# Optimization experiments

Measured on AMD Instinct MI355X. Metric: run time of the kernel, lower is better.

The kernel has to match this reference:

```python
import jax, jax.numpy as jnp
import numpy as np

N = 100000   # nodes
E = 1600000  # edges
B = 64       # graphs
NI, EI, GI = 64, 32, 32   # node_in, edge_in, global_in
NO, EO, GO = 32, 32, 32   # node_out, edge_out, global_out
H = 3                     # attention heads
NEG_SLOPE = 0.2


def setup_inputs() -> dict:
    key = jax.random.key(0)
    ks = jax.random.split(key, 20)
    s = 0.1
    return {
        # graph data
        "x": jax.random.normal(ks[0], (N, NI), jnp.float32),
        "edge_attr": jax.random.normal(ks[1], (E, EI), jnp.float32),
        "glob": jax.random.normal(ks[2], (B, GI), jnp.float32),
        # edge_mlp: Lin(node_in+edge_in, edge_out)
        "W_edge": jax.random.normal(ks[3], (NI + EI, EO), jnp.float32) * s,
        "b_edge": jax.random.normal(ks[4], (EO,), jnp.float32) * s,
        # GATv2Conv params (heads=3, edge_dim=EO)
        "W_l": jax.random.normal(ks[5], (NI, H * NO), jnp.float32) * s,
        "b_l": jax.random.normal(ks[6], (H * NO,), jnp.float32) * s,
        "W_r": jax.random.normal(ks[7], (NI, H * NO), jnp.float32) * s,
        "b_r": jax.random.normal(ks[8], (H * NO,), jnp.float32) * s,
        "W_e": jax.random.normal(ks[9], (EO, H * NO), jnp.float32) * s,   # lin_edge (no bias)
        "att": jax.random.normal(ks[10], (H, NO), jnp.float32) * s,
        "bias_gat": jax.random.normal(ks[11], (H * NO,), jnp.float32) * s,
        # node_mlp_2: Lin(node_out*3 + global_in, node_out)
        "W_n2": jax.random.normal(ks[12], (H * NO + GI, NO), jnp.float32) * s,
        "b_n2": jax.random.normal(ks[13], (NO,), jnp.float32) * s,
        # global_mlp: Lin(global_in + node_out, global_out)
        "W_g": jax.random.normal(ks[14], (GI + NO, GO), jnp.float32) * s,
        "b_g": jax.random.normal(ks[15], (GO,), jnp.float32) * s,
        # int inputs
        "edge_index": jax.random.randint(ks[16], (2, E), 0, N, jnp.int32),
        "batch": jnp.sort(jax.random.randint(ks[17], (N,), 0, B, jnp.int32)),
    }


def reference(x, edge_attr, glob, W_edge, b_edge, W_l, b_l, W_r, b_r, W_e,
              att, bias_gat, W_n2, b_n2, W_g, b_g, edge_index, batch):
    src, dst = edge_index[0], edge_index[1]

    # --- edge model: relu(Lin([x[src], edge_attr])) ---
    e = jax.nn.relu(jnp.concatenate([x[src], edge_attr], axis=1) @ W_edge + b_edge)  # [E, EO]

    # --- node model: GATv2Conv(heads=3, edge_dim=EO), concat heads ---
    xl = (x @ W_l + b_l).reshape(N, H, NO)   # source transform
    xr = (x @ W_r + b_r).reshape(N, H, NO)   # target transform
    m = xl[src] + xr[dst] + (e @ W_e).reshape(E, H, NO)          # [E,H,NO]
    logits = (jax.nn.leaky_relu(m, NEG_SLOPE) * att).sum(-1)     # [E,H]
    # segment softmax over incoming edges of each target node
    mx = jax.ops.segment_max(logits, dst, num_segments=N)        # [N,H]
    ex = jnp.exp(logits - mx[dst])
    den = jax.ops.segment_sum(ex, dst, num_segments=N)           # [N,H]
    alpha = ex / den[dst]                                        # [E,H]
    msg = (alpha[..., None] * xl[src]).reshape(E, H * NO)
    gat_out = jax.ops.segment_sum(msg, dst, num_segments=N) + bias_gat  # [N, H*NO]
    x_new = jax.nn.relu(jnp.concatenate([gat_out, glob[batch]], axis=1) @ W_n2 + b_n2)  # [N,NO]

    # --- global model: relu(Lin([glob, scatter_mean(x_new, batch)])) ---
    cnt = jax.ops.segment_sum(jnp.ones((N,), x.dtype), batch, num_segments=B)
    mean = jax.ops.segment_sum(x_new, batch, num_segments=B) / jnp.maximum(cnt, 1.0)[:, None]
    u_new = jax.nn.relu(jnp.concatenate([glob, mean], axis=1) @ W_g + b_g)  # [B,GO]

    return x_new, e, u_new
```

## Files before the change

kernel.cpp:

```cpp
#include <hip/hip_runtime.h>

#define N_NODES 100000
#define N_EDGES 1600000
#define NB 64
#define NI 64
#define EI 32
#define GI 32
#define NO 32
#define EO 32
#define GO 32
#define HH 3
#define HNO 96
#define NEG 0.2f
#define SCAN_BLKS 98

__global__ __launch_bounds__(256) void kA_node(
    const float* __restrict__ x,
    const float* __restrict__ W_l, const float* __restrict__ b_l,
    const float* __restrict__ W_r, const float* __restrict__ b_r,
    const float* __restrict__ W_edge, const float* __restrict__ b_edge,
    float* __restrict__ xl3, float* __restrict__ xr3, float* __restrict__ pre_e,
    int niters)
{
    __shared__ float sWl[NI * HNO];
    __shared__ float sWr[NI * HNO];
    __shared__ float sWp[NI * 32];
    __shared__ float sx[64 * NI];
    int t = threadIdx.x;
    for (int f = t; f < NI * HNO; f += 256) { sWl[f] = W_l[f]; sWr[f] = W_r[f]; }
    for (int f = t; f < NI * 32; f += 256) sWp[f] = W_edge[f];
    __syncthreads();
    int k = t & 31, g = t >> 5;
    float bl0 = b_l[k], bl1 = b_l[k + 32], bl2 = b_l[k + 64];
    float br0 = b_r[k], br1 = b_r[k + 32], br2 = b_r[k + 64];
    float bpe = b_edge[k];
    const long NX = (long)N_NODES * NI;
    for (int it = 0; it < niters; ++it) {
        long nb = ((long)blockIdx.x + (long)it * gridDim.x) * 64;
        long base = nb * NI;
        for (int f = t; f < 64 * NI; f += 256) {
            long idx = base + f;
            sx[f] = x[idx < NX ? idx : 0];
        }
        __syncthreads();
        float aL0[8], aL1[8], aL2[8], aR0[8], aR1[8], aR2[8], aP[8];
        #pragma unroll
        for (int m = 0; m < 8; ++m) {
            aL0[m] = bl0; aL1[m] = bl1; aL2[m] = bl2;
            aR0[m] = br0; aR1[m] = br1; aR2[m] = br2;
            aP[m] = bpe;
        }
        const float* sxg = &sx[g * 8 * NI];
        for (int i = 0; i < NI; ++i) {
            float wl0 = sWl[i * HNO + k], wl1 = sWl[i * HNO + 32 + k], wl2 = sWl[i * HNO + 64 + k];
            float wr0 = sWr[i * HNO + k], wr1 = sWr[i * HNO + 32 + k], wr2 = sWr[i * HNO + 64 + k];
            float wp  = sWp[i * 32 + k];
            #pragma unroll
            for (int m = 0; m < 8; ++m) {
                float xv = sxg[m * NI + i];
                aL0[m] += xv * wl0; aL1[m] += xv * wl1; aL2[m] += xv * wl2;
                aR0[m] += xv * wr0; aR1[m] += xv * wr1; aR2[m] += xv * wr2;
                aP[m]  += xv * wp;
            }
        }
        #pragma unroll
        for (int m = 0; m < 8; ++m) {
            long n = nb + g * 8 + m;
            if (n < N_NODES) {
                long b3 = n * HNO + (long)k * 3;
                xl3[b3]     = aL0[m];
                xl3[b3 + 1] = aL1[m];
                xl3[b3 + 2] = aL2[m];
                xr3[b3]     = aR0[m];
                xr3[b3 + 1] = aR1[m];
                xr3[b3 + 2] = aR2[m];
                pre_e[n * 32 + k] = aP[m];
            }
        }
        __syncthreads();
    }
}

__global__ __launch_bounds__(256) void k_hist(const int* __restrict__ eidx, int* __restrict__ cnt)
{
    long i = (long)blockIdx.x * 256 + threadIdx.x;
    long stride = (long)gridDim.x * 256;
    for (; i < N_EDGES; i += stride)
        atomicAdd(&cnt[eidx[N_EDGES + i]], 1);
}

__global__ __launch_bounds__(1024) void k_scan1(const int* __restrict__ cnt, int* __restrict__ bsum)
{
    __shared__ int s[1024];
    int i = blockIdx.x * 1024 + threadIdx.x;
    s[threadIdx.x] = (i < N_NODES) ? cnt[i] : 0;
    for (int o = 512; o > 0; o >>= 1) {
        __syncthreads();
        if (threadIdx.x < o) s[threadIdx.x] += s[threadIdx.x + o];
    }
    if (threadIdx.x == 0) bsum[blockIdx.x] = s[0];
}

__global__ __launch_bounds__(128) void k_scan2(int* __restrict__ bsum)
{
    __shared__ int s[128];
    int v = (threadIdx.x < SCAN_BLKS) ? bsum[threadIdx.x] : 0;
    s[threadIdx.x] = v;
    for (int o = 1; o < 128; o <<= 1) {
        __syncthreads();
        int a = (threadIdx.x >= o) ? s[threadIdx.x - o] : 0;
        __syncthreads();
        s[threadIdx.x] += a;
    }
    if (threadIdx.x < SCAN_BLKS) bsum[threadIdx.x] = s[threadIdx.x] - v;
}

__global__ __launch_bounds__(1024) void k_scan3(const int* __restrict__ cnt,
                                                const int* __restrict__ bsum,
                                                int* __restrict__ off, int* __restrict__ cursor)
{
    __shared__ int s[1024];
    int i = blockIdx.x * 1024 + threadIdx.x;
    int v = (i < N_NODES) ? cnt[i] : 0;
    s[threadIdx.x] = v;
    for (int o = 1; o < 1024; o <<= 1) {
        __syncthreads();
        int a = (threadIdx.x >= o) ? s[threadIdx.x - o] : 0;
        __syncthreads();
        s[threadIdx.x] += a;
    }
    int excl = bsum[blockIdx.x] + s[threadIdx.x] - v;
    if (i < N_NODES) {
        off[i] = excl; cursor[i] = excl;
        if (i == N_NODES - 1) off[N_NODES] = excl + v;
    }
}

__global__ __launch_bounds__(256) void k_scatter(const int* __restrict__ eidx,
                                                 int* __restrict__ cursor,
                                                 int2* __restrict__ ep)
{
    long i = (long)blockIdx.x * 256 + threadIdx.x;
    long stride = (long)gridDim.x * 256;
    for (; i < N_EDGES; i += stride) {
        int s = eidx[i];
        int d = eidx[N_EDGES + i];
        int pos = atomicAdd(&cursor[d], 1);
        ep[pos] = make_int2((int)i, s);
    }
}

__global__ __launch_bounds__(256) void kE_edge(
    const int* __restrict__ eidx, const float* __restrict__ pre_e,
    const float* __restrict__ ea, const float* __restrict__ W_edge,
    float* __restrict__ e_out, int niters)
{
    __shared__ float sW2[32 * 32];
    __shared__ float2 sEa2[8][32];
    int t = threadIdx.x;
    for (int f = t; f < 32 * 32; f += 256) sW2[f] = W_edge[64 * 32 + f];
    __syncthreads();
    int k = t & 31, gid = t >> 5;
    for (int it = 0; it < niters; ++it) {
        long e0 = ((long)blockIdx.x + (long)it * gridDim.x) * 16 + gid * 2;
        long e1 = e0 + 1;
        bool v0 = (e0 < N_EDGES), v1 = (e1 < N_EDGES);
        long c0 = v0 ? e0 : 0, c1 = v1 ? e1 : 0;
        int s0 = eidx[c0], s1 = eidx[c1];
        float acc0 = pre_e[(long)s0 * 32 + k];
        float acc1 = pre_e[(long)s1 * 32 + k];
        sEa2[gid][k] = make_float2(ea[c0 * EI + k], ea[c1 * EI + k]);
        #pragma unroll 8
        for (int i = 0; i < 32; ++i) {
            float w = sW2[i * 32 + k];
            float2 v = sEa2[gid][i];
            acc0 += v.x * w; acc1 += v.y * w;
        }
        if (v0) e_out[c0 * EO + k] = fmaxf(acc0, 0.f);
        if (v1) e_out[c1 * EO + k] = fmaxf(acc1, 0.f);
    }
}

__global__ __launch_bounds__(256) void kF(
    const float* __restrict__ eo_in, const float* __restrict__ W_e,
    const float* __restrict__ att,
    const float* __restrict__ xl3, const float* __restrict__ xr3,
    const int2* __restrict__ ep, const int* __restrict__ off,
    const float* __restrict__ bias_gat,
    float* __restrict__ g_out, int niters)
{
    __shared__ float sWeI[32 * 96];
    __shared__ float2 sEo2[8][32];
    int t = threadIdx.x;
    for (int f = t; f < 32 * 96; f += 256) {
        int i = f / 96, r = f - i * 96;
        int kk = r / 3, h = r - kk * 3;
        sWeI[f] = W_e[i * 96 + h * 32 + kk];
    }
    __syncthreads();
    int k = t & 31, gid = t >> 5;
    float at0 = att[k], at1 = att[32 + k], at2 = att[64 + k];
    float bg0 = bias_gat[k], bg1 = bias_gat[32 + k], bg2 = bias_gat[64 + k];
    const int k3 = k * 3;
    for (int it = 0; it < niters; ++it) {
        long n = ((long)blockIdx.x + (long)it * gridDim.x) * 8 + gid;
        if (n >= N_NODES) continue;
        int lo = off[n], hi = off[n + 1];
        long nb3 = n * HNO + k3;
        float xr0 = xr3[nb3], xr1 = xr3[nb3 + 1], xr2 = xr3[nb3 + 2];
        float a0 = 0.f, a1 = 0.f, a2 = 0.f;
        float d0 = 0.f, d1 = 0.f, d2 = 0.f;
        int deg = hi - lo;
        int steps = (deg + 1) >> 1;
        int eA = 0, sA = 0, eB = 0, sB = 0;
        int eA1 = 0, sA1 = 0, eB1 = 0, sB1 = 0;
        float eoAc = 0.f, eoBc = 0.f;
        float xlA0 = 0.f, xlA1 = 0.f, xlA2 = 0.f, xlB0 = 0.f, xlB1 = 0.f, xlB2 = 0.f;
        if (steps > 0) {
            int2 q = ep[lo]; eA = q.x; sA = q.y;
            if (lo + 1 < hi) { int2 r = ep[lo + 1]; eB = r.x; sB = r.y; }
            eoAc = eo_in[(long)eA * EO + k];
            eoBc = eo_in[(long)eB * EO + k];
            long a3 = (long)sA * HNO + k3, b3 = (long)sB * HNO + k3;
            xlA0 = xl3[a3]; xlA1 = xl3[a3 + 1]; xlA2 = xl3[a3 + 2];
            xlB0 = xl3[b3]; xlB1 = xl3[b3 + 1]; xlB2 = xl3[b3 + 2];
            if (lo + 2 < hi) { int2 q1 = ep[lo + 2]; eA1 = q1.x; sA1 = q1.y; }
            if (lo + 3 < hi) { int2 r1 = ep[lo + 3]; eB1 = r1.x; sB1 = r1.y; }
        }
        for (int st = 0; st < steps; ++st) {
            float eoA_n = eo_in[(long)eA1 * EO + k];
            float eoB_n = eo_in[(long)eB1 * EO + k];
            long a3 = (long)sA1 * HNO + k3, b3 = (long)sB1 * HNO + k3;
            float xlA0n = xl3[a3], xlA1n = xl3[a3 + 1], xlA2n = xl3[a3 + 2];
            float xlB0n = xl3[b3], xlB1n = xl3[b3 + 1], xlB2n = xl3[b3 + 2];
            int eA2 = 0, sA2 = 0, eB2 = 0, sB2 = 0;
            int pA2 = lo + 2 * st + 4;
            if (pA2 < hi)     { int2 q2 = ep[pA2];     eA2 = q2.x; sA2 = q2.y; }
            if (pA2 + 1 < hi) { int2 r2 = ep[pA2 + 1]; eB2 = r2.x; sB2 = r2.y; }
            sEo2[gid][k] = make_float2(eoAc, eoBc);
            float hA0 = xlA0 + xr0, hA1 = xlA1 + xr1, hA2 = xlA2 + xr2;
            float hB0 = xlB0 + xr0, hB1 = xlB1 + xr1, hB2 = xlB2 + xr2;
            #pragma unroll 8
            for (int i = 0; i < 32; ++i) {
                float2 ov = sEo2[gid][i];
                const float* wp = &sWeI[i * 96 + k3];
                float w0 = wp[0], w1 = wp[1], w2v = wp[2];
                hA0 += ov.x * w0; hA1 += ov.x * w1; hA2 += ov.x * w2v;
                hB0 += ov.y * w0; hB1 += ov.y * w1; hB2 += ov.y * w2v;
            }
            float pA0 = (hA0 > 0.f ? hA0 : NEG * hA0) * at0;
            float pA1 = (hA1 > 0.f ? hA1 : NEG * hA1) * at1;
            float pA2v = (hA2 > 0.f ? hA2 : NEG * hA2) * at2;
            float pB0 = (hB0 > 0.f ? hB0 : NEG * hB0) * at0;
            float pB1 = (hB1 > 0.f ? hB1 : NEG * hB1) * at1;
            float pB2 = (hB2 > 0.f ? hB2 : NEG * hB2) * at2;
            #pragma unroll
            for (int m = 1; m <= 16; m <<= 1) {
                pA0 += __shfl_xor(pA0, m, 32); pA1 += __shfl_xor(pA1, m, 32); pA2v += __shfl_xor(pA2v, m, 32);
                pB0 += __shfl_xor(pB0, m, 32); pB1 += __shfl_xor(pB1, m, 32); pB2 += __shfl_xor(pB2, m, 32);
            }
            bool okB = (lo + 2 * st + 1) < hi;
            float exA0 = __expf(pA0), exA1 = __expf(pA1), exA2 = __expf(pA2v);
            float exB0 = 0.f, exB1 = 0.f, exB2 = 0.f;
            if (okB) { exB0 = __expf(pB0); exB1 = __expf(pB1); exB2 = __expf(pB2); }
            a0 += exA0 * xlA0; a1 += exA1 * xlA1; a2 += exA2 * xlA2;
            a0 += exB0 * xlB0; a1 += exB1 * xlB1; a2 += exB2 * xlB2;
            d0 += exA0 + exB0; d1 += exA1 + exB1; d2 += exA2 + exB2;
            eA = eA1; sA = sA1; eB = eB1; sB = sB1;
            eA1 = eA2; sA1 = sA2; eB1 = eB2; sB1 = sB2;
            eoAc = eoA_n; eoBc = eoB_n;
            xlA0 = xlA0n; xlA1 = xlA1n; xlA2 = xlA2n;
            xlB0 = xlB0n; xlB1 = xlB1n; xlB2 = xlB2n;
        }
        g_out[n * HNO + k]      = (d0 > 0.f ? a0 / d0 : 0.f) + bg0;
        g_out[n * HNO + 32 + k] = (d1 > 0.f ? a1 / d1 : 0.f) + bg1;
        g_out[n * HNO + 64 + k] = (d2 > 0.f ? a2 / d2 : 0.f) + bg2;
    }
}

__global__ __launch_bounds__(256) void k2_node_out(
    const float* __restrict__ g, const float* __restrict__ glob,
    const int* __restrict__ batch, const float* __restrict__ W_n2,
    const float* __restrict__ b_n2, float* __restrict__ x_new, int niters)
{
    __shared__ float sW[128 * 32];
    __shared__ float sIn[8][128];
    int t = threadIdx.x;
    for (int f = t; f < 128 * 32; f += 256) sW[f] = W_n2[f];
    __syncthreads();
    int k = t & 31, ni = t >> 5;
    float bn = b_n2[k];
    for (int it = 0; it < niters; ++it) {
        long n = ((long)blockIdx.x + (long)it * gridDim.x) * 8 + ni;
        long nc = (n < N_NODES) ? n : 0;
        #pragma unroll
        for (int r = 0; r < 3; ++r) {
            int j = r * 32 + k;
            sIn[ni][j] = g[nc * HNO + j];
        }
        sIn[ni][96 + k] = glob[(long)batch[nc] * GI + k];
        __syncthreads();
        float acc = bn;
        #pragma unroll 8
        for (int i = 0; i < 128; ++i) acc += sIn[ni][i] * sW[i * 32 + k];
        if (n < N_NODES) x_new[n * NO + k] = fmaxf(acc, 0.f);
        __syncthreads();
    }
}

__device__ __forceinline__ int lower_bound_dev(const int* __restrict__ a, int n, int v) {
    int lo = 0, hi = n;
    while (lo < hi) { int mid = (lo + hi) >> 1; if (a[mid] < v) lo = mid + 1; else hi = mid; }
    return lo;
}

__global__ __launch_bounds__(256) void k3_global(
    const float* __restrict__ x_new, const int* __restrict__ batch,
    const float* __restrict__ glob, const float* __restrict__ W_g,
    const float* __restrict__ b_g, float* __restrict__ u_new)
{
    __shared__ int s_lo, s_hi;
    __shared__ float s_part[8][32];
    __shared__ float s_mean[32];
    int g = blockIdx.x;
    if (threadIdx.x == 0) {
        s_lo = lower_bound_dev(batch, N_NODES, g);
        s_hi = lower_bound_dev(batch, N_NODES, g + 1);
    }
    __syncthreads();
    int lo = s_lo, hi = s_hi;
    int k = threadIdx.x & 31, c = threadIdx.x >> 5;
    float acc = 0.f;
    for (long n = lo + c; n < hi; n += 8) acc += x_new[n * NO + k];
    s_part[c][k] = acc;
    __syncthreads();
    if (threadIdx.x < 32) {
        float s = 0.f;
        #pragma unroll
        for (int c2 = 0; c2 < 8; ++c2) s += s_part[c2][k];
        int cnt = hi - lo;
        s_mean[k] = s / (float)(cnt > 0 ? cnt : 1);
    }
    __syncthreads();
    if (threadIdx.x < 32) {
        float acc2 = b_g[k];
        #pragma unroll
        for (int i = 0; i < 32; ++i) acc2 += glob[g * GI + i] * W_g[i * GO + k];
        #pragma unroll
        for (int i = 0; i < 32; ++i) acc2 += s_mean[i] * W_g[(32 + i) * GO + k];
        u_new[g * GO + k] = fmaxf(acc2, 0.f);
    }
}

extern "C" void kernel_launch(void* const* d_in, const int* in_sizes, int n_in,
                              void* d_out, int out_size, void* d_ws, size_t ws_size,
                              hipStream_t stream) {
    const float* x        = (const float*)d_in[0];
    const float* edge_attr= (const float*)d_in[1];
    const float* glob     = (const float*)d_in[2];
    const float* W_edge   = (const float*)d_in[3];
    const float* b_edge   = (const float*)d_in[4];
    const float* W_l      = (const float*)d_in[5];
    const float* b_l      = (const float*)d_in[6];
    const float* W_r      = (const float*)d_in[7];
    const float* b_r      = (const float*)d_in[8];
    const float* W_e      = (const float*)d_in[9];
    const float* att      = (const float*)d_in[10];
    const float* bias_gat = (const float*)d_in[11];
    const float* W_n2     = (const float*)d_in[12];
    const float* b_n2     = (const float*)d_in[13];
    const float* W_g      = (const float*)d_in[14];
    const float* b_g      = (const float*)d_in[15];
    const int* edge_index = (const int*)d_in[16];
    const int* batch      = (const int*)d_in[17];

    float* out   = (float*)d_out;
    float* x_new = out;
    float* e_out = out + (size_t)N_NODES * NO;
    float* u_new = e_out + (size_t)N_EDGES * EO;

    float*  ws    = (float*)d_ws;
    float*  xl3   = ws;
    float*  xr3   = xl3 + (size_t)N_NODES * HNO;
    float*  pre_e = xr3 + (size_t)N_NODES * HNO;
    float*  g_buf = pre_e + (size_t)N_NODES * 32;
    int2*   ep    = (int2*)(g_buf + (size_t)N_NODES * HNO);
    int*    cnt   = (int*)(ep + (size_t)N_EDGES);
    int*    off   = cnt + N_NODES;
    int*    cursor= off + N_NODES + 1;
    int*    bsum  = cursor + N_NODES;

    hipMemsetAsync(cnt, 0, (size_t)N_NODES * sizeof(int), stream);

    k_hist<<<1024, 256, 0, stream>>>(edge_index, cnt);
    k_scan1<<<SCAN_BLKS, 1024, 0, stream>>>(cnt, bsum);
    k_scan2<<<1, 128, 0, stream>>>(bsum);
    k_scan3<<<SCAN_BLKS, 1024, 0, stream>>>(cnt, bsum, off, cursor);
    k_scatter<<<1024, 256, 0, stream>>>(edge_index, cursor, ep);

    int gridA = 1024;
    int groups64 = (N_NODES + 63) / 64;
    int itA = (groups64 + gridA - 1) / gridA;
    kA_node<<<gridA, 256, 0, stream>>>(x, W_l, b_l, W_r, b_r, W_edge, b_edge,
                                       xl3, xr3, pre_e, itA);

    int gridE = 2048;
    int groupsE = (N_EDGES + 15) / 16;
    int itE = (groupsE + gridE - 1) / gridE;
    kE_edge<<<gridE, 256, 0, stream>>>(edge_index, pre_e, edge_attr, W_edge, e_out, itE);

    int gridF = 2048;
    int groups8 = (N_NODES + 7) / 8;
    int itF = (groups8 + gridF - 1) / gridF;
    kF<<<gridF, 256, 0, stream>>>(e_out, W_e, att, xl3, xr3,
                                  ep, off, bias_gat, g_buf, itF);

    int grid2 = 1024;
    int it2 = (groups8 + grid2 - 1) / grid2;
    k2_node_out<<<grid2, 256, 0, stream>>>(g_buf, glob, batch, W_n2, b_n2, x_new, it2);

    k3_global<<<NB, 256, 0, stream>>>(x_new, batch, glob, W_g, b_g, u_new);
}
```

Before: 1.286 ms.

## Fuse histogram into node kernel, scatter into edge kernel, node MLP into GAT

Measured after the change: 1.255 ms. 2.4% less time.

```diff
diff --git a/kernel.cpp b/kernel.cpp
--- a/kernel.cpp
+++ b/kernel.cpp
@@ -15,7 +15,7 @@
 #define SCAN_BLKS 98
 
 __global__ __launch_bounds__(256) void kA_node(
-    const float* __restrict__ x,
+    const float* __restrict__ x, const int* __restrict__ eidx, int* __restrict__ cnt,
     const float* __restrict__ W_l, const float* __restrict__ b_l,
     const float* __restrict__ W_r, const float* __restrict__ b_r,
     const float* __restrict__ W_edge, const float* __restrict__ b_edge,
@@ -27,6 +27,12 @@
     __shared__ float sWp[NI * 32];
     __shared__ float sx[64 * NI];
     int t = threadIdx.x;
+    {
+        long i = (long)blockIdx.x * 256 + t;
+        long stride = (long)gridDim.x * 256;
+        for (; i < N_EDGES; i += stride)
+            atomicAdd(&cnt[eidx[N_EDGES + i]], 1);
+    }
     for (int f = t; f < NI * HNO; f += 256) { sWl[f] = W_l[f]; sWr[f] = W_r[f]; }
     for (int f = t; f < NI * 32; f += 256) sWp[f] = W_edge[f];
     __syncthreads();
@@ -81,14 +87,6 @@
     }
 }
 
-__global__ __launch_bounds__(256) void k_hist(const int* __restrict__ eidx, int* __restrict__ cnt)
-{
-    long i = (long)blockIdx.x * 256 + threadIdx.x;
-    long stride = (long)gridDim.x * 256;
-    for (; i < N_EDGES; i += stride)
-        atomicAdd(&cnt[eidx[N_EDGES + i]], 1);
-}
-
 __global__ __launch_bounds__(1024) void k_scan1(const int* __restrict__ cnt, int* __restrict__ bsum)
 {
     __shared__ int s[1024];
@@ -136,24 +134,10 @@
     }
 }
 
-__global__ __launch_bounds__(256) void k_scatter(const int* __restrict__ eidx,
-                                                 int* __restrict__ cursor,
-                                                 int2* __restrict__ ep)
-{
-    long i = (long)blockIdx.x * 256 + threadIdx.x;
-    long stride = (long)gridDim.x * 256;
-    for (; i < N_EDGES; i += stride) {
-        int s = eidx[i];
-        int d = eidx[N_EDGES + i];
-        int pos = atomicAdd(&cursor[d], 1);
-        ep[pos] = make_int2((int)i, s);
-    }
-}
-
-__global__ __launch_bounds__(256) void kE_edge(
-    const int* __restrict__ eidx, const float* __restrict__ pre_e,
-    const float* __restrict__ ea, const float* __restrict__ W_edge,
-    float* __restrict__ e_out, int niters)
+__global__ __launch_bounds__(256) void kEscat(
+    const int* __restrict__ eidx, int* __restrict__ cursor, int2* __restrict__ ep,
+    const float* __restrict__ pre_e, const float* __restrict__ ea,
+    const float* __restrict__ W_edge, float* __restrict__ e_out, int niters)
 {
     __shared__ float sW2[32 * 32];
     __shared__ float2 sEa2[8][32];
@@ -167,6 +151,16 @@
         bool v0 = (e0 < N_EDGES), v1 = (e1 < N_EDGES);
         long c0 = v0 ? e0 : 0, c1 = v1 ? e1 : 0;
         int s0 = eidx[c0], s1 = eidx[c1];
+        if (k < 2) {
+            bool vv = (k == 0) ? v0 : v1;
+            if (vv) {
+                long ce = (k == 0) ? c0 : c1;
+                int ss = (k == 0) ? s0 : s1;
+                int dd = eidx[N_EDGES + ce];
+                int pos = atomicAdd(&cursor[dd], 1);
+                ep[pos] = make_int2((int)ce, ss);
+            }
+        }
         float acc0 = pre_e[(long)s0 * 32 + k];
         float acc1 = pre_e[(long)s1 * 32 + k];
         sEa2[gid][k] = make_float2(ea[c0 * EI + k], ea[c1 * EI + k]);
@@ -186,21 +180,27 @@
     const float* __restrict__ att,
     const float* __restrict__ xl3, const float* __restrict__ xr3,
     const int2* __restrict__ ep, const int* __restrict__ off,
-    const float* __restrict__ bias_gat,
-    float* __restrict__ g_out, int niters)
+    const float* __restrict__ bias_gat, const float* __restrict__ glob,
+    const int* __restrict__ batch, const float* __restrict__ W_n2,
+    const float* __restrict__ b_n2,
+    float* __restrict__ x_new, int niters)
 {
     __shared__ float sWeI[32 * 96];
     __shared__ float2 sEo2[8][32];
+    __shared__ float sWn[128 * 32];
+    __shared__ float sG[8][128];
     int t = threadIdx.x;
     for (int f = t; f < 32 * 96; f += 256) {
         int i = f / 96, r = f - i * 96;
         int kk = r / 3, h = r - kk * 3;
         sWeI[f] = W_e[i * 96 + h * 32 + kk];
     }
+    for (int f = t; f < 128 * 32; f += 256) sWn[f] = W_n2[f];
     __syncthreads();
     int k = t & 31, gid = t >> 5;
     float at0 = att[k], at1 = att[32 + k], at2 = att[64 + k];
     float bg0 = bias_gat[k], bg1 = bias_gat[32 + k], bg2 = bias_gat[64 + k];
+    float bn = b_n2[k];
     const int k3 = k * 3;
     for (int it = 0; it < niters; ++it) {
         long n = ((long)blockIdx.x + (long)it * gridDim.x) * 8 + gid;
@@ -272,39 +272,15 @@
             xlA0 = xlA0n; xlA1 = xlA1n; xlA2 = xlA2n;
             xlB0 = xlB0n; xlB1 = xlB1n; xlB2 = xlB2n;
         }
-        g_out[n * HNO + k]      = (d0 > 0.f ? a0 / d0 : 0.f) + bg0;
-        g_out[n * HNO + 32 + k] = (d1 > 0.f ? a1 / d1 : 0.f) + bg1;
-        g_out[n * HNO + 64 + k] = (d2 > 0.f ? a2 / d2 : 0.f) + bg2;
-    }
-}
-
-__global__ __launch_bounds__(256) void k2_node_out(
-    const float* __restrict__ g, const float* __restrict__ glob,
-    const int* __restrict__ batch, const float* __restrict__ W_n2,
-    const float* __restrict__ b_n2, float* __restrict__ x_new, int niters)
-{
-    __shared__ float sW[128 * 32];
-    __shared__ float sIn[8][128];
-    int t = threadIdx.x;
-    for (int f = t; f < 128 * 32; f += 256) sW[f] = W_n2[f];
-    __syncthreads();
-    int k = t & 31, ni = t >> 5;
-    float bn = b_n2[k];
-    for (int it = 0; it < niters; ++it) {
-        long n = ((long)blockIdx.x + (long)it * gridDim.x) * 8 + ni;
-        long nc = (n < N_NODES) ? n : 0;
-        #pragma unroll
-        for (int r = 0; r < 3; ++r) {
-            int j = r * 32 + k;
-            sIn[ni][j] = g[nc * HNO + j];
-        }
-        sIn[ni][96 + k] = glob[(long)batch[nc] * GI + k];
-        __syncthreads();
-        float acc = bn;
+        float g0 = (d0 > 0.f ? a0 / d0 : 0.f) + bg0;
+        float g1 = (d1 > 0.f ? a1 / d1 : 0.f) + bg1;
+        float g2 = (d2 > 0.f ? a2 / d2 : 0.f) + bg2;
+        float gg = glob[(long)batch[n] * GI + k];
+        sG[gid][k] = g0; sG[gid][32 + k] = g1; sG[gid][64 + k] = g2; sG[gid][96 + k] = gg;
+        float acc2 = bn;
         #pragma unroll 8
-        for (int i = 0; i < 128; ++i) acc += sIn[ni][i] * sW[i * 32 + k];
-        if (n < N_NODES) x_new[n * NO + k] = fmaxf(acc, 0.f);
-        __syncthreads();
+        for (int i = 0; i < 128; ++i) acc2 += sG[gid][i] * sWn[i * 32 + k];
+        x_new[n * NO + k] = fmaxf(acc2, 0.f);
     }
 }
 
@@ -383,8 +359,7 @@
     float*  xl3   = ws;
     float*  xr3   = xl3 + (size_t)N_NODES * HNO;
     float*  pre_e = xr3 + (size_t)N_NODES * HNO;
-    float*  g_buf = pre_e + (size_t)N_NODES * 32;
-    int2*   ep    = (int2*)(g_buf + (size_t)N_NODES * HNO);
+    int2*   ep    = (int2*)(pre_e + (size_t)N_NODES * 32);
     int*    cnt   = (int*)(ep + (size_t)N_EDGES);
     int*    off   = cnt + N_NODES;
     int*    cursor= off + N_NODES + 1;
@@ -392,32 +367,28 @@
 
     hipMemsetAsync(cnt, 0, (size_t)N_NODES * sizeof(int), stream);
 
-    k_hist<<<1024, 256, 0, stream>>>(edge_index, cnt);
+    int gridA = 1024;
+    int groups64 = (N_NODES + 63) / 64;
+    int itA = (groups64 + gridA - 1) / gridA;
+    kA_node<<<gridA, 256, 0, stream>>>(x, edge_index, cnt, W_l, b_l, W_r, b_r,
+                                       W_edge, b_edge, xl3, xr3, pre_e, itA);
+
     k_scan1<<<SCAN_BLKS, 1024, 0, stream>>>(cnt, bsum);
     k_scan2<<<1, 128, 0, stream>>>(bsum);
     k_scan3<<<SCAN_BLKS, 1024, 0, stream>>>(cnt, bsum, off, cursor);
-    k_scatter<<<1024, 256, 0, stream>>>(edge_index, cursor, ep);
-
-    int gridA = 1024;
-    int groups64 = (N_NODES + 63) / 64;
-    int itA = (groups64 + gridA - 1) / gridA;
-    kA_node<<<gridA, 256, 0, stream>>>(x, W_l, b_l, W_r, b_r, W_edge, b_edge,
-                                       xl3, xr3, pre_e, itA);
 
     int gridE = 2048;
     int groupsE = (N_EDGES + 15) / 16;
     int itE = (groupsE + gridE - 1) / gridE;
-    kE_edge<<<gridE, 256, 0, stream>>>(edge_index, pre_e, edge_attr, W_edge, e_out, itE);
+    kEscat<<<gridE, 256, 0, stream>>>(edge_index, cursor, ep, pre_e, edge_attr,
+                                      W_edge, e_out, itE);
 
     int gridF = 2048;
     int groups8 = (N_NODES + 7) / 8;
     int itF = (groups8 + gridF - 1) / gridF;
     kF<<<gridF, 256, 0, stream>>>(e_out, W_e, att, xl3, xr3,
-                                  ep, off, bias_gat, g_buf, itF);
-
-    int grid2 = 1024;
-    int it2 = (groups8 + grid2 - 1) / grid2;
-    k2_node_out<<<grid2, 256, 0, stream>>>(g_buf, glob, batch, W_n2, b_n2, x_new, it2);
+                                  ep, off, bias_gat, glob, batch, W_n2, b_n2,
+                                  x_new, itF);
 
     k3_global<<<NB, 256, 0, stream>>>(x_new, batch, glob, W_g, b_g, u_new);
 }
```
